# Kernel optimization log

Measured on AMD Instinct MI355X. Metric: run time of the kernel, lower is better.

## Reference

```python
import jax, jax.numpy as jnp
import numpy as np

D_MODEL = 1024
N_HEADS = 16
HEAD_DIM = D_MODEL // N_HEADS


def setup_inputs() -> dict:
    key = jax.random.key(0)
    ks = jax.random.split(key, 12)
    B, S = 2, 2048
    scale = 1.0 / np.sqrt(D_MODEL)
    inp = {
        "query": jax.random.normal(ks[0], (B, S, D_MODEL), jnp.float32),
        "key": jax.random.normal(ks[1], (B, S, D_MODEL), jnp.float32),
        "value": jax.random.normal(ks[2], (B, S, D_MODEL), jnp.float32),
        "Wq": jax.random.normal(ks[3], (D_MODEL, D_MODEL), jnp.float32) * scale,
        "bq": jnp.zeros((D_MODEL,), jnp.float32),
        "Wk": jax.random.normal(ks[4], (D_MODEL, D_MODEL), jnp.float32) * scale,
        "bk": jnp.zeros((D_MODEL,), jnp.float32),
        "Wv": jax.random.normal(ks[5], (D_MODEL, D_MODEL), jnp.float32) * scale,
        "bv": jnp.zeros((D_MODEL,), jnp.float32),
        "Wo": jax.random.normal(ks[6], (D_MODEL, D_MODEL), jnp.float32) * scale,
        "bo": jnp.zeros((D_MODEL,), jnp.float32),
    }
    return inp


def _split_heads(x):
    # [B, S, D] -> [B, H, S, Dh]
    B, S, _ = x.shape
    return x.reshape(B, S, N_HEADS, HEAD_DIM).transpose(0, 2, 1, 3)


def reference(query, key, value, Wq, bq, Wk, bk, Wv, bv, Wo, bo):
    B, S, _ = query.shape
    Q = _split_heads(query @ Wq + bq)   # [B,H,S,Dh]
    K = _split_heads(key @ Wk + bk)
    V = _split_heads(value @ Wv + bv)
    inv_sqrt_dh = 1.0 / np.sqrt(HEAD_DIM).astype(np.float32)
    scores = jnp.einsum("bhqd,bhkd->bhqk", Q, K) * inv_sqrt_dh
    attention = jax.nn.softmax(scores, axis=-1)
    # dropout is identity in eval mode
    out = jnp.einsum("bhqk,bhkd->bhqd", attention, V)
    out = out.transpose(0, 2, 1, 3).reshape(B, S, D_MODEL)
    out = out @ Wo + bo
    return out, attention
```

## Files before the change

### kernel.cpp

```cpp
#include <hip/hip_runtime.h>
#include <math.h>

#define D_MODEL 1024
#define NHEADS 16
#define HDIM 64
#define BATCH 2
#define SEQ 2048
#define MROWS (BATCH * SEQ)

typedef unsigned int uint32;
typedef __attribute__((ext_vector_type(8))) short short8;
typedef __attribute__((ext_vector_type(4))) float f32x4;
typedef __attribute__((ext_vector_type(16))) float f32x16;
typedef __attribute__((ext_vector_type(2))) unsigned int uint2v;

__device__ __forceinline__ unsigned short f2bf(float f) {
  unsigned int u = __float_as_uint(f);
  u += 0x7fffu + ((u >> 16) & 1u);
  return (unsigned short)(u >> 16);
}

__device__ __forceinline__ float fexp2(float x) {
  float r;
  asm("v_exp_f32 %0, %1" : "=v"(r) : "v"(x));
  return r;
}

__device__ __forceinline__ float flog2(float x) {
  float r;
  asm("v_log_f32 %0, %1" : "=v"(r) : "v"(x));
  return r;
}

__device__ __forceinline__ unsigned int cvtpk(float lo, float hi) {
  unsigned int r;
  asm("v_cvt_pk_bf16_f32 %0, %1, %2" : "=v"(r) : "v"(lo), "v"(hi));
  return r;
}

__device__ __forceinline__ void bar_lgkm() {
  asm volatile("s_waitcnt lgkmcnt(0)\n\ts_barrier" ::: "memory");
}

__device__ __forceinline__ void gl_lds16(const void* g, void* l) {
  __builtin_amdgcn_global_load_lds((const __attribute__((address_space(1))) void*)g,
                                   (__attribute__((address_space(3))) void*)l, 16, 0, 0);
}

struct PrepArgs {
  const float* act[3];
  unsigned short* actout[3];
  const float* w[4];
  unsigned short* wout;
};

__global__ __launch_bounds__(256) void prep_kernel(PrepArgs args) {
  int bid = blockIdx.x;
  int t = threadIdx.x;
  if (bid < 6144) {
    int z = bid >> 11, blk = bid & 2047;
    const float* s = args.act[z];
    unsigned short* d = args.actout[z];
    int i = (blk * 256 + t) * 8;
    float4 v0 = *(const float4*)(s + i);
    float4 v1 = *(const float4*)(s + i + 4);
    uint4 o;
    o.x = cvtpk(v0.x, v0.y);
    o.y = cvtpk(v0.z, v0.w);
    o.z = cvtpk(v1.x, v1.y);
    o.w = cvtpk(v1.z, v1.w);
    *(uint4*)(d + i) = o;
  } else {
    __shared__ unsigned short tile[64][80];
    int wb = bid - 6144;
    int zz = wb >> 8, rem = wb & 255;
    int n0 = (rem & 15) * 64, k0 = (rem >> 4) * 64;
    const float* W = args.w[zz];
    unsigned short* WT = args.wout + (size_t)zz * (D_MODEL * D_MODEL);
    int r = t >> 2, cc = (t & 3) * 16;
    const float* src = W + (size_t)(k0 + r) * D_MODEL + n0 + cc;
#pragma unroll
    for (int j = 0; j < 16; j += 4) {
      float4 v = *(const float4*)(src + j);
      tile[r][cc + j + 0] = f2bf(v.x);
      tile[r][cc + j + 1] = f2bf(v.y);
      tile[r][cc + j + 2] = f2bf(v.z);
      tile[r][cc + j + 3] = f2bf(v.w);
    }
    __syncthreads();
    __align__(16) unsigned short tmp[16];
#pragma unroll
    for (int j = 0; j < 16; ++j) tmp[j] = tile[cc + j][r];
    unsigned short* d = WT + (size_t)(n0 + r) * D_MODEL + k0 + cc;
    *(uint4*)d = ((uint4*)tmp)[0];
    *(uint4*)(d + 8) = ((uint4*)tmp)[1];
  }
}

struct GemmArgs {
  const unsigned short* A[3];
  const unsigned short* W[3];
  const float* bias[3];
  void* C[3];
};

#define GEMM_BODY(A_, B_)                                                              \
  for (int kt = 0; kt < D_MODEL; kt += 64) {                                           \
    _Pragma("unroll") for (int i = 0; i < 4; ++i) {                                    \
      int row = wave * 32 + i * 8;                                                     \
      gl_lds16(A_ + (size_t)(m0 + row + r8) * D_MODEL + kt + c8, As + row * 64);       \
    }                                                                                  \
    _Pragma("unroll") for (int i = 0; i < 2; ++i) {                                    \
      int row = wave * 16 + i * 8;                                                     \
      gl_lds16(B_ + (size_t)(n0 + row + r8) * D_MODEL + kt + c8, Bs + row * 64);       \
    }                                                                                  \
    __syncthreads();                                                                   \
    short8 af[4][2], bf[2][2];                                                         \
    _Pragma("unroll") for (int f = 0; f < 4; ++f)                                      \
      _Pragma("unroll") for (int kk = 0; kk < 2; ++kk)                                 \
        af[f][kk] = *(const short8*)((const char*)As + (wm + f * 16 + lr) * 128 +      \
                                     kk * 64 + lg * 16);                               \
    _Pragma("unroll") for (int j = 0; j < 2; ++j)                                      \
      _Pragma("unroll") for (int kk = 0; kk < 2; ++kk)                                 \
        bf[j][kk] = *(const short8*)((const char*)Bs + (wn + j * 16 + lr) * 128 +      \
                                     kk * 64 + lg * 16);                               \
    _Pragma("unroll") for (int i = 0; i < 4; ++i)                                      \
      _Pragma("unroll") for (int j = 0; j < 2; ++j)                                    \
        _Pragma("unroll") for (int kk = 0; kk < 2; ++kk)                               \
          acc[i][j] = __builtin_amdgcn_mfma_f32_16x16x32_bf16(af[i][kk], bf[j][kk],    \
                                                              acc[i][j], 0, 0, 0);     \
    __syncthreads();                                                                   \
  }

__global__ __launch_bounds__(256) void gemm_qkv_kernel(GemmArgs args) {
  int bid = blockIdx.x;
  int wgid = (bid & 7) * 192 + (bid >> 3);
  const unsigned short *A, *WT;
  const float* bias;
  void* C;
  int m0, n0;
  bool vtrans;
  if (wgid < 1024) {
    int z = wgid >> 9, rem = wgid & 511;
    int x = rem & 15, y = rem >> 4;
    A = args.A[z]; WT = args.W[z]; bias = args.bias[z]; C = args.C[z];
    n0 = x * 64; m0 = y * 128; vtrans = false;
  } else {
    int rem = wgid - 1024;
    int x2 = rem & 63, y2 = rem >> 6;
    A = args.W[2];
    WT = args.A[2];
    bias = args.bias[2]; C = args.C[2];
    n0 = x2 * 64; m0 = y2 * 128; vtrans = true;
  }
  __shared__ __align__(16) unsigned short As[128 * 64];
  __shared__ __align__(16) unsigned short Bs[64 * 64];
  int t = threadIdx.x;
  int wave = t >> 6, lane = t & 63;
  int wm = (wave >> 1) * 64, wn = (wave & 1) * 32;
  int lr = lane & 15, lg = lane >> 4;
  int r8 = lane >> 3, c8 = (lane & 7) * 8;
  f32x4 acc[4][2] = {};

  GEMM_BODY(A, WT)

  if (!vtrans) {
#pragma unroll
    for (int i = 0; i < 4; ++i)
#pragma unroll
      for (int j = 0; j < 2; ++j) {
        int col = n0 + wn + j * 16 + lr;
        float bb = bias[col];
#pragma unroll
        for (int r = 0; r < 4; ++r) {
          int row = m0 + wm + i * 16 + lg * 4 + r;
          ((unsigned short*)C)[(size_t)row * D_MODEL + col] = f2bf(acc[i][j][r] + bb);
        }
      }
  } else {
#pragma unroll
    for (int i = 0; i < 4; ++i)
#pragma unroll
      for (int j = 0; j < 2; ++j) {
        int col = n0 + wn + j * 16 + lr;
#pragma unroll
        for (int r = 0; r < 4; ++r) {
          int row = m0 + wm + i * 16 + lg * 4 + r;
          ((unsigned short*)C)[(size_t)row * MROWS + col] = f2bf(acc[i][j][r] + bias[row]);
        }
      }
  }
}

__global__ __launch_bounds__(512) void attn_kernel(const unsigned short* Q, const unsigned short* K,
                                                   const unsigned short* Vt2, float* attn,
                                                   unsigned short* ctx) {
  int bid = blockIdx.x;
  int wgid = (bid & 7) * 32 + (bid >> 3);
  int bh = wgid >> 3;
  int q0 = (wgid & 7) * 256;
  int b = bh >> 4, h = bh & 15;
  int t = threadIdx.x, wave = t >> 6, lane = t & 63;
  int l31 = lane & 31, hi = lane >> 5;

  __shared__ __align__(16) char Ks[2][64 * 128];
  __shared__ __align__(16) char Vs[2][64 * 128];

  const unsigned short* Kp = K + (size_t)(b * SEQ) * D_MODEL + h * HDIM;
  const unsigned short* Vp = Vt2 + (size_t)(h * HDIM) * MROWS + b * SEQ;

  int srow = t >> 3, sch = t & 7;
  int scb = (sch * 16) ^ ((srow & 7) << 4);

  short8 qv[4];
  {
    const unsigned short* qp = Q + (size_t)(b * SEQ + q0 + wave * 32 + l31) * D_MODEL + h * HDIM + hi * 8;
#pragma unroll
    for (int kk = 0; kk < 4; ++kk) qv[kk] = *(const short8*)(qp + kk * 16);
  }

  const float SCL = 0.125f * 1.44269504f;
  float lsum = 0.f;
  f32x16 oacc[2] = {};

  {
    *(uint4*)(Ks[0] + srow * 128 + scb) = *(const uint4*)(Kp + (size_t)srow * D_MODEL + sch * 8);
    *(uint4*)(Vs[0] + srow * 128 + scb) = *(const uint4*)(Vp + (size_t)srow * MROWS + sch * 8);
  }
  bar_lgkm();
  int cur = 0;
  for (int ti = 0; ti < 32; ++ti) {
    uint4 nk, nv;
    bool more = (ti + 1) < 32;
    if (more) {
      nk = *(const uint4*)(Kp + (size_t)((ti + 1) * 64 + srow) * D_MODEL + sch * 8);
      nv = *(const uint4*)(Vp + (size_t)srow * MROWS + (ti + 1) * 64 + sch * 8);
    }
    f32x16 st[2] = {};
#pragma unroll
    for (int n = 0; n < 2; ++n)
#pragma unroll
      for (int kk = 0; kk < 4; ++kk) {
        int kr = n * 32 + l31;
        short8 ak = *(const short8*)(Ks[cur] + kr * 128 + ((kk * 32 + hi * 16) ^ ((kr & 7) << 4)));
        st[n] = __builtin_amdgcn_mfma_f32_32x32x16_bf16(ak, qv[kk], st[n], 0, 0, 0);
      }
    unsigned int P0[2][4], P1[2][4];
#pragma unroll
    for (int n = 0; n < 2; ++n)
#pragma unroll
      for (int j2 = 0; j2 < 4; ++j2) {
        float p0 = fexp2(st[n][4 * j2 + 0] * SCL);
        float p1 = fexp2(st[n][4 * j2 + 1] * SCL);
        float p2 = fexp2(st[n][4 * j2 + 2] * SCL);
        float p3 = fexp2(st[n][4 * j2 + 3] * SCL);
        lsum += (p0 + p1) + (p2 + p3);
        P0[n][j2] = cvtpk(p0, p1);
        P1[n][j2] = cvtpk(p2, p3);
      }
    short8 pa[4];
#pragma unroll
    for (int n = 0; n < 2; ++n)
#pragma unroll
      for (int c = 0; c < 2; ++c) {
        uint2v s0 = __builtin_amdgcn_permlane32_swap(P0[n][2 * c], P0[n][2 * c + 1], false, false);
        uint2v s1 = __builtin_amdgcn_permlane32_swap(P1[n][2 * c], P1[n][2 * c + 1], false, false);
        uint4 w;
        w.x = s0.x; w.y = s1.x; w.z = s0.y; w.w = s1.y;
        pa[n * 2 + c] = *(short8*)&w;
      }
#pragma unroll
    for (int n2 = 0; n2 < 2; ++n2)
#pragma unroll
      for (int kk = 0; kk < 4; ++kk) {
        int vr = n2 * 32 + l31;
        short8 bv = *(const short8*)(Vs[cur] + vr * 128 + ((kk * 32 + hi * 16) ^ ((vr & 7) << 4)));
        oacc[n2] = __builtin_amdgcn_mfma_f32_32x32x16_bf16(pa[kk], bv, oacc[n2], 0, 0, 0);
      }
    if (more) {
      *(uint4*)(Ks[cur ^ 1] + srow * 128 + scb) = nk;
      *(uint4*)(Vs[cur ^ 1] + srow * 128 + scb) = nv;
    }
    bar_lgkm();
    cur ^= 1;
  }
  float tot = lsum + __shfl_xor(lsum, 32, 64);
  float inv = 1.f / tot;
  float iv16[16];
#pragma unroll
  for (int reg = 0; reg < 16; ++reg) {
    int qr = (reg & 3) + 8 * (reg >> 2) + 4 * hi;
    iv16[reg] = __shfl(inv, qr, 64);
  }
#pragma unroll
  for (int n2 = 0; n2 < 2; ++n2)
#pragma unroll
    for (int reg = 0; reg < 16; ++reg) {
      int qr = (reg & 3) + 8 * (reg >> 2) + 4 * hi;
      int row = b * SEQ + q0 + wave * 32 + qr;
      ctx[(size_t)row * D_MODEL + h * HDIM + n2 * 32 + l31] = f2bf(oacc[n2][reg] * iv16[reg]);
    }

  float* rowp[16];
  float l2iv[16];
  {
    float* abase = attn + (size_t)bh * SEQ * SEQ + l31;
#pragma unroll
    for (int reg = 0; reg < 16; ++reg) {
      int qr = (reg & 3) + 8 * (reg >> 2) + 4 * hi;
      rowp[reg] = abase + (size_t)(q0 + wave * 32 + qr) * SEQ;
      l2iv[reg] = flog2(iv16[reg]);
    }
  }
  {
    *(uint4*)(Ks[0] + srow * 128 + scb) = *(const uint4*)(Kp + (size_t)srow * D_MODEL + sch * 8);
  }
  bar_lgkm();
  cur = 0;
  for (int ti = 0; ti < 32; ++ti) {
    uint4 nk;
    bool more = (ti + 1) < 32;
    if (more) {
      nk = *(const uint4*)(Kp + (size_t)((ti + 1) * 64 + srow) * D_MODEL + sch * 8);
    }
    f32x16 st[2] = {};
#pragma unroll
    for (int n = 0; n < 2; ++n)
#pragma unroll
      for (int kk = 0; kk < 4; ++kk) {
        int kr = n * 32 + l31;
        short8 bk = *(const short8*)(Ks[cur] + kr * 128 + ((kk * 32 + hi * 16) ^ ((kr & 7) << 4)));
        st[n] = __builtin_amdgcn_mfma_f32_32x32x16_bf16(qv[kk], bk, st[n], 0, 0, 0);
      }
#pragma unroll
    for (int n = 0; n < 2; ++n)
#pragma unroll
      for (int reg = 0; reg < 16; ++reg) {
        float p = fexp2(fmaf(st[n][reg], SCL, l2iv[reg]));
        __builtin_nontemporal_store(p, rowp[reg] + ti * 64 + n * 32);
      }
    if (more) {
      *(uint4*)(Ks[cur ^ 1] + srow * 128 + scb) = nk;
    }
    bar_lgkm();
    cur ^= 1;
  }
}

__global__ __launch_bounds__(256) void gemm_o_kernel(const unsigned short* A, const unsigned short* WT,
                                                     const float* bias, float* C) {
  int bid = blockIdx.x;
  int wgid = (bid & 7) * 64 + (bid >> 3);
  int x = wgid & 15, y = wgid >> 4;
  int n0 = x * 64, m0 = y * 128;
  __shared__ __align__(16) unsigned short As[128 * 64];
  __shared__ __align__(16) unsigned short Bs[64 * 64];
  int t = threadIdx.x;
  int wave = t >> 6, lane = t & 63;
  int wm = (wave >> 1) * 64, wn = (wave & 1) * 32;
  int lr = lane & 15, lg = lane >> 4;
  int r8 = lane >> 3, c8 = (lane & 7) * 8;
  f32x4 acc[4][2] = {};

  GEMM_BODY(A, WT)

#pragma unroll
  for (int i = 0; i < 4; ++i)
#pragma unroll
    for (int j = 0; j < 2; ++j) {
      int col = n0 + wn + j * 16 + lr;
      float bb = bias[col];
#pragma unroll
      for (int r = 0; r < 4; ++r) {
        int row = m0 + wm + i * 16 + lg * 4 + r;
        C[(size_t)row * D_MODEL + col] = acc[i][j][r] + bb;
      }
    }
}

extern "C" void kernel_launch(void* const* d_in, const int* in_sizes, int n_in,
                              void* d_out, int out_size, void* d_ws, size_t ws_size,
                              hipStream_t stream) {
  const float* query = (const float*)d_in[0];
  const float* key   = (const float*)d_in[1];
  const float* value = (const float*)d_in[2];
  const float* Wq = (const float*)d_in[3];
  const float* bq = (const float*)d_in[4];
  const float* Wk = (const float*)d_in[5];
  const float* bk = (const float*)d_in[6];
  const float* Wv = (const float*)d_in[7];
  const float* bv = (const float*)d_in[8];
  const float* Wo = (const float*)d_in[9];
  const float* bo = (const float*)d_in[10];

  char* ws = (char*)d_ws;
  const size_t MB = (size_t)1 << 20;
  unsigned short* WqT = (unsigned short*)(ws + 0 * MB);
  unsigned short* WvT = (unsigned short*)(ws + 4 * MB);
  unsigned short* WoT = (unsigned short*)(ws + 6 * MB);
  unsigned short* Xq  = (unsigned short*)(ws + 8 * MB);
  unsigned short* Xk  = (unsigned short*)(ws + 16 * MB);
  unsigned short* Xv  = (unsigned short*)(ws + 24 * MB);
  unsigned short* Qw  = (unsigned short*)(ws + 32 * MB);
  unsigned short* Kw  = (unsigned short*)(ws + 40 * MB);
  unsigned short* Vt2 = (unsigned short*)(ws + 48 * MB);
  unsigned short* Cw  = (unsigned short*)(ws + 8 * MB);

  float* out0 = (float*)d_out;
  float* attn = out0 + (size_t)MROWS * D_MODEL;

  PrepArgs pa;
  pa.act[0] = query; pa.act[1] = key; pa.act[2] = value;
  pa.actout[0] = Xq; pa.actout[1] = Xk; pa.actout[2] = Xv;
  pa.w[0] = Wq; pa.w[1] = Wk; pa.w[2] = Wv; pa.w[3] = Wo;
  pa.wout = WqT;
  prep_kernel<<<dim3(7168), 256, 0, stream>>>(pa);

  GemmArgs ga;
  ga.A[0] = Xq; ga.A[1] = Xk; ga.A[2] = Xv;
  ga.W[0] = WqT; ga.W[1] = WqT + (size_t)D_MODEL * D_MODEL; ga.W[2] = WvT;
  ga.bias[0] = bq; ga.bias[1] = bk; ga.bias[2] = bv;
  ga.C[0] = Qw; ga.C[1] = Kw; ga.C[2] = Vt2;
  gemm_qkv_kernel<<<dim3(1536), 256, 0, stream>>>(ga);

  attn_kernel<<<dim3(256), 512, 0, stream>>>(Qw, Kw, Vt2, attn, Cw);

  gemm_o_kernel<<<dim3(512), 256, 0, stream>>>(Cw, WoT, bo, out0);
}
```

Before: 250.8 us.

## Split attention-probability write into fused kernel co-scheduled with output projection

```diff
diff --git a/kernel.cpp b/kernel.cpp
--- a/kernel.cpp
+++ b/kernel.cpp
@@ -192,9 +192,9 @@
   }
 }
 
-__global__ __launch_bounds__(512) void attn_kernel(const unsigned short* Q, const unsigned short* K,
-                                                   const unsigned short* Vt2, float* attn,
-                                                   unsigned short* ctx) {
+__global__ __launch_bounds__(512) void attn_ctx_kernel(const unsigned short* Q, const unsigned short* K,
+                                                       const unsigned short* Vt2, float* invl_g,
+                                                       unsigned short* ctx) {
   int bid = blockIdx.x;
   int wgid = (bid & 7) * 32 + (bid >> 3);
   int bh = wgid >> 3;
@@ -286,6 +286,7 @@
   }
   float tot = lsum + __shfl_xor(lsum, 32, 64);
   float inv = 1.f / tot;
+  if (lane < 32) invl_g[(size_t)bh * SEQ + q0 + wave * 32 + l31] = inv;
   float iv16[16];
 #pragma unroll
   for (int reg = 0; reg < 16; ++reg) {
@@ -300,82 +301,141 @@
       int row = b * SEQ + q0 + wave * 32 + qr;
       ctx[(size_t)row * D_MODEL + h * HDIM + n2 * 32 + l31] = f2bf(oacc[n2][reg] * iv16[reg]);
     }
-
-  float* rowp[16];
-  float l2iv[16];
-  {
-    float* abase = attn + (size_t)bh * SEQ * SEQ + l31;
-#pragma unroll
-    for (int reg = 0; reg < 16; ++reg) {
-      int qr = (reg & 3) + 8 * (reg >> 2) + 4 * hi;
-      rowp[reg] = abase + (size_t)(q0 + wave * 32 + qr) * SEQ;
-      l2iv[reg] = flog2(iv16[reg]);
-    }
-  }
-  {
-    *(uint4*)(Ks[0] + srow * 128 + scb) = *(const uint4*)(Kp + (size_t)srow * D_MODEL + sch * 8);
-  }
-  bar_lgkm();
-  cur = 0;
-  for (int ti = 0; ti < 32; ++ti) {
-    uint4 nk;
-    bool more = (ti + 1) < 32;
-    if (more) {
-      nk = *(const uint4*)(Kp + (size_t)((ti + 1) * 64 + srow) * D_MODEL + sch * 8);
-    }
-    f32x16 st[2] = {};
-#pragma unroll
-    for (int n = 0; n < 2; ++n)
-#pragma unroll
-      for (int kk = 0; kk < 4; ++kk) {
-        int kr = n * 32 + l31;
-        short8 bk = *(const short8*)(Ks[cur] + kr * 128 + ((kk * 32 + hi * 16) ^ ((kr & 7) << 4)));
-        st[n] = __builtin_amdgcn_mfma_f32_32x32x16_bf16(qv[kk], bk, st[n], 0, 0, 0);
-      }
-#pragma unroll
-    for (int n = 0; n < 2; ++n)
-#pragma unroll
-      for (int reg = 0; reg < 16; ++reg) {
-        float p = fexp2(fmaf(st[n][reg], SCL, l2iv[reg]));
-        __builtin_nontemporal_store(p, rowp[reg] + ti * 64 + n * 32);
-      }
-    if (more) {
-      *(uint4*)(Ks[cur ^ 1] + srow * 128 + scb) = nk;
-    }
-    bar_lgkm();
-    cur ^= 1;
-  }
-}
-
-__global__ __launch_bounds__(256) void gemm_o_kernel(const unsigned short* A, const unsigned short* WT,
-                                                     const float* bias, float* C) {
+}
+
+__global__ __launch_bounds__(512) void fat_kernel(const unsigned short* Q, const unsigned short* K,
+                                                  const float* invl_g, float* attn,
+                                                  const unsigned short* Cw, const unsigned short* WoT,
+                                                  const float* bias, float* out0) {
+  __shared__ __align__(16) char smem[49152];
   int bid = blockIdx.x;
   int wgid = (bid & 7) * 64 + (bid >> 3);
-  int x = wgid & 15, y = wgid >> 4;
-  int n0 = x * 64, m0 = y * 128;
-  __shared__ __align__(16) unsigned short As[128 * 64];
-  __shared__ __align__(16) unsigned short Bs[64 * 64];
-  int t = threadIdx.x;
-  int wave = t >> 6, lane = t & 63;
-  int wm = (wave >> 1) * 64, wn = (wave & 1) * 32;
-  int lr = lane & 15, lg = lane >> 4;
-  int r8 = lane >> 3, c8 = (lane & 7) * 8;
-  f32x4 acc[4][2] = {};
-
-  GEMM_BODY(A, WT)
-
-#pragma unroll
-  for (int i = 0; i < 4; ++i)
-#pragma unroll
-    for (int j = 0; j < 2; ++j) {
-      int col = n0 + wn + j * 16 + lr;
-      float bb = bias[col];
-#pragma unroll
-      for (int r = 0; r < 4; ++r) {
-        int row = m0 + wm + i * 16 + lg * 4 + r;
-        C[(size_t)row * D_MODEL + col] = acc[i][j][r] + bb;
-      }
-    }
+  int t = threadIdx.x, wave = t >> 6, lane = t & 63;
+
+  if (wgid < 256) {
+    int bh = wgid >> 3;
+    int q0 = (wgid & 7) * 256;
+    int b = bh >> 4, h = bh & 15;
+    int l31 = lane & 31, hi = lane >> 5;
+    char* Ks0 = smem;
+    char* Ks1 = smem + 64 * 128;
+
+    const unsigned short* Kp = K + (size_t)(b * SEQ) * D_MODEL + h * HDIM;
+    int srow = t >> 3, sch = t & 7;
+    int scb = (sch * 16) ^ ((srow & 7) << 4);
+
+    short8 qv[4];
+    {
+      const unsigned short* qp = Q + (size_t)(b * SEQ + q0 + wave * 32 + l31) * D_MODEL + h * HDIM + hi * 8;
+#pragma unroll
+      for (int kk = 0; kk < 4; ++kk) qv[kk] = *(const short8*)(qp + kk * 16);
+    }
+    const float SCL = 0.125f * 1.44269504f;
+    float* rowp[16];
+    float l2iv[16];
+    {
+      float* abase = attn + (size_t)bh * SEQ * SEQ + l31;
+      const float* ivb = invl_g + (size_t)bh * SEQ + q0 + wave * 32;
+#pragma unroll
+      for (int reg = 0; reg < 16; ++reg) {
+        int qr = (reg & 3) + 8 * (reg >> 2) + 4 * hi;
+        rowp[reg] = abase + (size_t)(q0 + wave * 32 + qr) * SEQ;
+        l2iv[reg] = flog2(ivb[qr]);
+      }
+    }
+    {
+      *(uint4*)(Ks0 + srow * 128 + scb) = *(const uint4*)(Kp + (size_t)srow * D_MODEL + sch * 8);
+    }
+    bar_lgkm();
+    int cur = 0;
+    for (int ti = 0; ti < 32; ++ti) {
+      uint4 nk;
+      bool more = (ti + 1) < 32;
+      if (more) {
+        nk = *(const uint4*)(Kp + (size_t)((ti + 1) * 64 + srow) * D_MODEL + sch * 8);
+      }
+      char* Kc = cur ? Ks1 : Ks0;
+      f32x16 st[2] = {};
+#pragma unroll
+      for (int n = 0; n < 2; ++n)
+#pragma unroll
+        for (int kk = 0; kk < 4; ++kk) {
+          int kr = n * 32 + l31;
+          short8 bk = *(const short8*)(Kc + kr * 128 + ((kk * 32 + hi * 16) ^ ((kr & 7) << 4)));
+          st[n] = __builtin_amdgcn_mfma_f32_32x32x16_bf16(qv[kk], bk, st[n], 0, 0, 0);
+        }
+#pragma unroll
+      for (int n = 0; n < 2; ++n)
+#pragma unroll
+        for (int reg = 0; reg < 16; ++reg) {
+          float p = fexp2(fmaf(st[n][reg], SCL, l2iv[reg]));
+          __builtin_nontemporal_store(p, rowp[reg] + ti * 64 + n * 32);
+        }
+      if (more) {
+        char* Kn = cur ? Ks0 : Ks1;
+        *(uint4*)(Kn + srow * 128 + scb) = nk;
+      }
+      bar_lgkm();
+      cur ^= 1;
+    }
+  } else {
+    int idx = wgid - 256;
+    int half = wave >> 2, wave4 = wave & 3;
+    int tile_id = idx * 2 + half;
+    int x = tile_id & 15, y = tile_id >> 4;
+    int n0 = x * 64, m0 = y * 128;
+    unsigned short* As = (unsigned short*)(smem + half * 24576);
+    unsigned short* Bs = (unsigned short*)(smem + half * 24576 + 16384);
+    int wm = (wave4 >> 1) * 64, wn = (wave4 & 1) * 32;
+    int lr = lane & 15, lg = lane >> 4;
+    int r8 = lane >> 3, c8 = (lane & 7) * 8;
+    f32x4 acc[4][2] = {};
+
+    for (int kt = 0; kt < D_MODEL; kt += 64) {
+#pragma unroll
+      for (int i = 0; i < 4; ++i) {
+        int row = wave4 * 32 + i * 8;
+        gl_lds16(Cw + (size_t)(m0 + row + r8) * D_MODEL + kt + c8, As + row * 64);
+      }
+#pragma unroll
+      for (int i = 0; i < 2; ++i) {
+        int row = wave4 * 16 + i * 8;
+        gl_lds16(WoT + (size_t)(n0 + row + r8) * D_MODEL + kt + c8, Bs + row * 64);
+      }
+      __syncthreads();
+      short8 af[4][2], bf[2][2];
+#pragma unroll
+      for (int f = 0; f < 4; ++f)
+#pragma unroll
+        for (int kk = 0; kk < 2; ++kk)
+          af[f][kk] = *(const short8*)((const char*)As + (wm + f * 16 + lr) * 128 + kk * 64 + lg * 16);
+#pragma unroll
+      for (int j = 0; j < 2; ++j)
+#pragma unroll
+        for (int kk = 0; kk < 2; ++kk)
+          bf[j][kk] = *(const short8*)((const char*)Bs + (wn + j * 16 + lr) * 128 + kk * 64 + lg * 16);
+#pragma unroll
+      for (int i = 0; i < 4; ++i)
+#pragma unroll
+        for (int j = 0; j < 2; ++j)
+#pragma unroll
+          for (int kk = 0; kk < 2; ++kk)
+            acc[i][j] = __builtin_amdgcn_mfma_f32_16x16x32_bf16(af[i][kk], bf[j][kk], acc[i][j], 0, 0, 0);
+      __syncthreads();
+    }
+#pragma unroll
+    for (int i = 0; i < 4; ++i)
+#pragma unroll
+      for (int j = 0; j < 2; ++j) {
+        int col = n0 + wn + j * 16 + lr;
+        float bb = bias[col];
+#pragma unroll
+        for (int r = 0; r < 4; ++r) {
+          int row = m0 + wm + i * 16 + lg * 4 + r;
+          out0[(size_t)row * D_MODEL + col] = acc[i][j][r] + bb;
+        }
+      }
+  }
 }
 
 extern "C" void kernel_launch(void* const* d_in, const int* in_sizes, int n_in,
@@ -405,6 +465,7 @@
   unsigned short* Kw  = (unsigned short*)(ws + 40 * MB);
   unsigned short* Vt2 = (unsigned short*)(ws + 48 * MB);
   unsigned short* Cw  = (unsigned short*)(ws + 8 * MB);
+  float* invl_g       = (float*)(ws + 16 * MB);
 
   float* out0 = (float*)d_out;
   float* attn = out0 + (size_t)MROWS * D_MODEL;
@@ -423,7 +484,7 @@
   ga.C[0] = Qw; ga.C[1] = Kw; ga.C[2] = Vt2;
   gemm_qkv_kernel<<<dim3(1536), 256, 0, stream>>>(ga);
 
-  attn_kernel<<<dim3(256), 512, 0, stream>>>(Qw, Kw, Vt2, attn, Cw);
-
-  gemm_o_kernel<<<dim3(512), 256, 0, stream>>>(Cw, WoT, bo, out0);
-}
+  attn_ctx_kernel<<<dim3(256), 512, 0, stream>>>(Qw, Kw, Vt2, invl_g, Cw);
+
+  fat_kernel<<<dim3(512), 512, 0, stream>>>(Qw, Kw, invl_g, attn, Cw, WoT, bo, out0);
+}
```

Result: slower. 268.4 us (+7.0%).
